# Kernel tuning notes

Measured on AMD Instinct MI355X. Metric: run time of the kernel, lower is better.

Reference implementation:

```python
import jax, jax.numpy as jnp
import numpy as np
from jax import lax

N_KERNELS = 11
N_GRAMS = 3
EMB = 300
CONV_OUT = 128
B, QLEN, DLEN = 128, 30, 256


def _kernel_mus(n):
    mus = [1.0]
    bin_size = 2.0 / (n - 1)
    mus.append(1 - bin_size / 2)
    for i in range(1, n - 1):
        mus.append(mus[i] - bin_size)
    return mus


def _kernel_sigmas(n):
    bin_size = 2.0 / (n - 1)
    return [0.001] + [0.5 * bin_size] * (n - 1)


MU = jnp.asarray(np.array(_kernel_mus(N_KERNELS), dtype=np.float32))      # [K]
SIGMA = jnp.asarray(np.array(_kernel_sigmas(N_KERNELS), dtype=np.float32))  # [K]


def setup_inputs() -> dict:
    key = jax.random.key(0)
    ks = jax.random.split(key, 10)
    inp = {
        "query_embeddings": jax.random.normal(ks[0], (B, QLEN, EMB), jnp.float32),
        "document_embeddings": jax.random.normal(ks[1], (B, DLEN, EMB), jnp.float32),
        "query_pad_oov_mask": jnp.ones((B, QLEN), jnp.float32),
        "document_pad_oov_mask": jnp.ones((B, DLEN), jnp.float32),
    }
    # conv weights for n-gram sizes 1..3: [out_ch, in_ch, ksize]
    for i in range(1, N_GRAMS + 1):
        inp[f"conv_w{i}"] = jax.random.normal(ks[1 + i], (CONV_OUT, EMB, i), jnp.float32) * 0.05
        inp[f"conv_b{i}"] = jnp.zeros((CONV_OUT,), jnp.float32)
    inp["dense_w"] = jax.random.uniform(ks[9], (1, N_KERNELS * N_GRAMS * N_GRAMS), jnp.float32,
                                        minval=-0.014, maxval=0.014)
    return inp


def _conv_ngram(x, w, b):
    # x: [B, L, E]; w: [C, E, k]; right-pad by k-1 so output length == L (ConstantPad1d((0,k-1)))
    k = w.shape[-1]
    y = lax.conv_general_dilated(x.transpose(0, 2, 1), w, (1,), [(0, k - 1)],
                                 dimension_numbers=("NCH", "OIH", "NCH"))
    return jax.nn.relu(y + b[None, :, None]).transpose(0, 2, 1)  # [B, L, C]


def _kernel_pool(q, d, qd_mask, q_mask):
    # cosine matrix (AllenNLP CosineMatrixAttention: normalize with +1e-13 eps)
    qn = q / (jnp.linalg.norm(q, axis=-1, keepdims=True) + 1e-13)
    dn = d / (jnp.linalg.norm(d, axis=-1, keepdims=True) + 1e-13)
    cos = jnp.einsum("bqe,bde->bqd", qn, dn) * qd_mask  # [B, Q, D]
    # RBF soft-histogram kernels: [B, Q, D, K]
    k = jnp.exp(-(cos[..., None] - MU) ** 2 / (2.0 * SIGMA ** 2)) * qd_mask[..., None]
    per_kernel_query = k.sum(axis=2)  # [B, Q, K]
    log_pk = jnp.log(jnp.clip(per_kernel_query, 1e-10, None)) * 0.01
    return (log_pk * q_mask[..., None]).sum(axis=1)  # [B, K]


def reference(query_embeddings, document_embeddings, query_pad_oov_mask, document_pad_oov_mask,
              conv_w1, conv_b1, conv_w2, conv_b2, conv_w3, conv_b3, dense_w):
    qd_mask = query_pad_oov_mask[:, :, None] * document_pad_oov_mask[:, None, :]  # [B, Q, D]
    conv_params = [(conv_w1, conv_b1), (conv_w2, conv_b2), (conv_w3, conv_b3)]
    q_res = [_conv_ngram(query_embeddings, w, b) for w, b in conv_params]
    d_res = [_conv_ngram(document_embeddings, w, b) for w, b in conv_params]
    matched = [_kernel_pool(q_res[i], d_res[t], qd_mask, query_pad_oov_mask)
               for i in range(N_GRAMS) for t in range(N_GRAMS)]
    all_grams = jnp.concatenate(matched, axis=1)  # [B, K*9]
    return jnp.squeeze(all_grams @ dense_w.T, axis=1)  # [B]
```

## Files before the change

kernel.cpp:

```cpp
#include <hip/hip_runtime.h>
#include <math.h>


typedef __bf16 bf16x8 __attribute__((ext_vector_type(8)));
typedef float f32x4 __attribute__((ext_vector_type(4)));

#if __has_builtin(__builtin_amdgcn_exp2f)
#define EXP2F(x) __builtin_amdgcn_exp2f(x)
#else
#define EXP2F(x) exp2f(x)
#endif

static __device__ __forceinline__ unsigned short f2bf(float f) {
  union { float f; unsigned int u; } v; v.f = f;
  unsigned int r = v.u + 0x7FFFu + ((v.u >> 16) & 1u);
  return (unsigned short)(r >> 16);
}

__global__ __launch_bounds__(256) void prep_w(
    const float* __restrict__ w1, const float* __restrict__ w2,
    const float* __restrict__ w3, unsigned short* __restrict__ wt2) {
  int idx = blockIdx.x * 256 + threadIdx.x;
  if (idx >= 245760) return;
  int jj   = idx & 7;
  int lane = (idx >> 3) & 63;
  int ec   = (idx >> 9) % 10;
  int cb   = (idx / 5120) & 7;
  int p    = idx / 40960;
  const float* w; int k, jt;
  if (p == 0)      { w = w1; k = 1; jt = 0; }
  else if (p <= 2) { w = w2; k = 2; jt = p - 1; }
  else             { w = w3; k = 3; jt = p - 3; }
  int c = cb * 16 + (lane & 15);
  int e = ec * 32 + (lane >> 4) * 8 + jj;
  float v = (e < 300) ? w[(c * 300 + e) * k + jt] : 0.0f;
  wt2[idx] = f2bf(v);
}

__device__ __forceinline__ constexpr int bIndex(int ni, int j) {
  constexpr int base[6] = {0, 1, 2, 4, 6, 9};
  return base[ni] + j;
}

template<int MI>
__device__ __forceinline__ void conv_body(
    unsigned short* As, float (*ssq)[64],
    const float* __restrict__ x, int L, int l0, int b,
    const unsigned short* __restrict__ wt2,
    const float* __restrict__ b1, const float* __restrict__ b2,
    const float* __restrict__ b3,
    unsigned short* __restrict__ out) {
  constexpr int ROWS = MI * 16 + 2;
  const int t = threadIdx.x;
  const int w = __builtin_amdgcn_readfirstlane(t >> 6);
  const int lane = t & 63;
  const int quad = lane >> 4, lrow = lane & 15;

  if (t < 192) ssq[t >> 6][t & 63] = 0.0f;

  const float* xb = x + (size_t)b * L * 300;
  for (int idx = t; idx < ROWS * 80; idx += 256) {
    int r = idx / 80, e4 = idx % 80;
    int e = e4 * 4;
    int l = l0 + r;
    float4 v = make_float4(0.f, 0.f, 0.f, 0.f);
    if (l < L && e < 300) v = *reinterpret_cast<const float4*>(xb + l * 300 + e);
    unsigned int lo = (unsigned int)f2bf(v.x) | ((unsigned int)f2bf(v.y) << 16);
    unsigned int hi = (unsigned int)f2bf(v.z) | ((unsigned int)f2bf(v.w) << 16);
    *reinterpret_cast<uint2*>(&As[r * 328 + e]) = make_uint2(lo, hi);
  }
  __syncthreads();

  const float* biases[3] = {b1, b2, b3};
  float bv[6];
  #pragma unroll
  for (int ni = 0; ni < 6; ++ni)
    bv[ni] = biases[ni >> 1][((ni & 1) * 4 + w) * 16 + lrow];

  f32x4 acc[MI][6];
  #pragma unroll
  for (int mi = 0; mi < MI; ++mi)
    #pragma unroll
    for (int ni = 0; ni < 6; ++ni) acc[mi][ni] = (f32x4){0.f, 0.f, 0.f, 0.f};

  const unsigned short* wl = wt2 + lane * 8;

  auto loadB = [&](int ec, bf16x8* dst) {
    #pragma unroll
    for (int ni = 0; ni < 6; ++ni) {
      const int g = ni >> 1;
      const int cb = (ni & 1) * 4 + w;
      const int pst = (g * (g + 1)) >> 1;
      #pragma unroll
      for (int j = 0; j <= g; ++j)
        dst[bIndex(ni, j)] = *reinterpret_cast<const bf16x8*>(
            wl + ((((pst + j) * 8 + cb) * 10 + ec) << 9));
    }
  };

  auto compute = [&](int ec, const bf16x8* B) {
    #pragma unroll
    for (int j = 0; j < 3; ++j) {
      bf16x8 af[MI];
      #pragma unroll
      for (int mi = 0; mi < MI; ++mi)
        af[mi] = *reinterpret_cast<const bf16x8*>(
            &As[(mi * 16 + lrow + j) * 328 + ec * 32 + quad * 8]);
      #pragma unroll
      for (int ni = 0; ni < 6; ++ni) {
        const int g = ni >> 1;
        if (j <= g) {
          #pragma unroll
          for (int mi = 0; mi < MI; ++mi)
            acc[mi][ni] = __builtin_amdgcn_mfma_f32_16x16x32_bf16(
                af[mi], B[bIndex(ni, j)], acc[mi][ni], 0, 0, 0);
        }
      }
    }
  };

  bf16x8 Bc[12], Bn[12];
  loadB(0, Bc);
  #pragma unroll
  for (int e2 = 0; e2 < 5; ++e2) {
    loadB(2 * e2 + 1, Bn);
    compute(2 * e2, Bc);
    if (e2 < 4) loadB(2 * e2 + 2, Bc);
    compute(2 * e2 + 1, Bn);
  }

  #pragma unroll
  for (int mi = 0; mi < MI; ++mi) {
    #pragma unroll
    for (int r = 0; r < 4; ++r) {
      #pragma unroll
      for (int g = 0; g < 3; ++g) {
        float y0 = fmaxf(acc[mi][2 * g + 0][r] + bv[2 * g + 0], 0.f);
        float y1 = fmaxf(acc[mi][2 * g + 1][r] + bv[2 * g + 1], 0.f);
        float p = y0 * y0 + y1 * y1;
        p += __shfl_xor(p, 1); p += __shfl_xor(p, 2);
        p += __shfl_xor(p, 4); p += __shfl_xor(p, 8);
        if (lrow == 0) atomicAdd(&ssq[g][mi * 16 + quad * 4 + r], p);
      }
    }
  }
  __syncthreads();

  #pragma unroll
  for (int mi = 0; mi < MI; ++mi) {
    #pragma unroll
    for (int r = 0; r < 4; ++r) {
      int row = mi * 16 + quad * 4 + r;
      int l = l0 + row;
      if (l < L) {
        #pragma unroll
        for (int g = 0; g < 3; ++g) {
          float inv = 1.0f / (sqrtf(ssq[g][row]) + 1e-13f);
          #pragma unroll
          for (int h = 0; h < 2; ++h) {
            int ni = 2 * g + h;
            int ch = ((ni & 1) * 4 + w) * 16 + lrow;
            float y = fmaxf(acc[mi][ni][r] + bv[ni], 0.f);
            out[((size_t)(g * 128 + b) * L + l) * 128 + ch] = f2bf(y * inv);
          }
        }
      }
    }
  }
}

__global__ __launch_bounds__(256) void conv_all(
    const float* __restrict__ qemb, const float* __restrict__ demb,
    const unsigned short* __restrict__ wt2,
    const float* __restrict__ b1, const float* __restrict__ b2,
    const float* __restrict__ b3,
    unsigned short* __restrict__ qn, unsigned short* __restrict__ dn) {
  __shared__ unsigned short As[66 * 328];
  __shared__ float ssq[3][64];
  const int bi = blockIdx.x;
  if (bi < 512)
    conv_body<4>(As, ssq, demb, 256, (bi & 3) * 64, bi >> 2, wt2, b1, b2, b3, dn);
  else
    conv_body<2>(As, ssq, qemb, 30, 0, bi - 512, wt2, b1, b2, b3, qn);
}

__global__ __launch_bounds__(64) void pool_mfma(
    const unsigned short* __restrict__ qn, const unsigned short* __restrict__ dn,
    const float* __restrict__ qmask, const float* __restrict__ dmask,
    float* __restrict__ pkq4) {
  const float MU[11] = {1.0f, 0.9f, 0.7f, 0.5f, 0.3f, 0.1f,
                        -0.1f, -0.3f, -0.5f, -0.7f, -0.9f};
  const float NEGC[11] = {-721347.52f, -72.134752f, -72.134752f, -72.134752f,
                          -72.134752f, -72.134752f, -72.134752f, -72.134752f,
                          -72.134752f, -72.134752f, -72.134752f};
  const int tg    = blockIdx.x >> 2;
  const int chunk = blockIdx.x & 3;
  const int b     = blockIdx.y;
  const int lane  = threadIdx.x;
  const int quad  = lane >> 4, l15 = lane & 15;
  const int d0    = chunk * 64;

  const unsigned short* dslab = dn + (size_t)(tg * 128 + b) * 256 * 128;

  bf16x8 aD[4][4];
  #pragma unroll
  for (int mi = 0; mi < 4; ++mi)
    #pragma unroll
    for (int kt = 0; kt < 4; ++kt)
      aD[mi][kt] = *reinterpret_cast<const bf16x8*>(
          dslab + (size_t)(d0 + mi * 16 + l15) * 128 + kt * 32 + quad * 8);

  float dmv[4][4];
  #pragma unroll
  for (int mi = 0; mi < 4; ++mi)
    #pragma unroll
    for (int r = 0; r < 4; ++r)
      dmv[mi][r] = dmask[b * 256 + d0 + mi * 16 + quad * 4 + r];

  float qmv[2];
  qmv[0] = qmask[b * 30 + l15];
  qmv[1] = (16 + l15 < 30) ? qmask[b * 30 + 16 + l15] : 0.0f;

  #pragma unroll 1
  for (int ig = 0; ig < 3; ++ig) {
    const unsigned short* qslab = qn + (size_t)(ig * 128 + b) * 30 * 128;

    bf16x8 bQ[2][4];
    #pragma unroll
    for (int ni = 0; ni < 2; ++ni)
      #pragma unroll
      for (int kt = 0; kt < 4; ++kt)
        bQ[ni][kt] = *reinterpret_cast<const bf16x8*>(
            qslab + (size_t)(ni * 16 + l15) * 128 + kt * 32 + quad * 8);

    f32x4 acc[4][2];
    #pragma unroll
    for (int mi = 0; mi < 4; ++mi)
      #pragma unroll
      for (int ni = 0; ni < 2; ++ni) acc[mi][ni] = (f32x4){0.f, 0.f, 0.f, 0.f};

    #pragma unroll
    for (int kt = 0; kt < 4; ++kt)
      #pragma unroll
      for (int mi = 0; mi < 4; ++mi)
        #pragma unroll
        for (int ni = 0; ni < 2; ++ni)
          acc[mi][ni] = __builtin_amdgcn_mfma_f32_16x16x32_bf16(
              aD[mi][kt], bQ[ni][kt], acc[mi][ni], 0, 0, 0);

    float feat[2][11];
    #pragma unroll
    for (int ni = 0; ni < 2; ++ni)
      #pragma unroll
      for (int kk = 0; kk < 11; ++kk) feat[ni][kk] = 0.0f;

    #pragma unroll
    for (int mi = 0; mi < 4; ++mi) {
      #pragma unroll
      for (int r = 0; r < 4; ++r) {
        #pragma unroll
        for (int ni = 0; ni < 2; ++ni) {
          float m  = qmv[ni] * dmv[mi][r];
          float cm = acc[mi][ni][r] * m;
          #pragma unroll
          for (int kk = 0; kk < 11; ++kk) {
            float d2 = cm - MU[kk];
            feat[ni][kk] += EXP2F(d2 * d2 * NEGC[kk]) * m;
          }
        }
      }
    }

    #pragma unroll
    for (int ni = 0; ni < 2; ++ni)
      #pragma unroll
      for (int kk = 0; kk < 11; ++kk) {
        float v = feat[ni][kk];
        v += __shfl_xor(v, 16);
        v += __shfl_xor(v, 32);
        feat[ni][kk] = v;
      }

    if (quad == 0) {
      const int pair = ig * 3 + tg;
      #pragma unroll
      for (int ni = 0; ni < 2; ++ni) {
        int q = ni * 16 + l15;
        if (q < 30) {
          float* p = pkq4 +
              (((size_t)(chunk * 9 + pair) * 128 + b) * 30 + q) * 11;
          #pragma unroll
          for (int kk = 0; kk < 11; ++kk) p[kk] = feat[ni][kk];
        }
      }
    }
  }
}

__global__ __launch_bounds__(128) void final_kernel(
    const float* __restrict__ pkq4, const float* __restrict__ qmask,
    const float* __restrict__ dw, float* __restrict__ out) {
  const int CH = 9 * 128 * 30 * 11;
  const int b = blockIdx.x;
  const int t = threadIdx.x;
  float s = 0.0f;
  for (int idx = t; idx < 9 * 30 * 11; idx += 128) {
    int pair = idx / 330;
    int rem  = idx % 330;
    int q    = rem / 11;
    int kk   = rem % 11;
    size_t base = (((size_t)pair * 128 + b) * 30 + q) * 11 + kk;
    float v = pkq4[base] + pkq4[base + CH] + pkq4[base + 2 * CH] +
              pkq4[base + 3 * CH];
    s += __logf(fmaxf(v, 1e-10f)) * 0.01f * qmask[b * 30 + q] * dw[pair * 11 + kk];
  }
  s += __shfl_xor(s, 1);  s += __shfl_xor(s, 2);  s += __shfl_xor(s, 4);
  s += __shfl_xor(s, 8);  s += __shfl_xor(s, 16); s += __shfl_xor(s, 32);
  __shared__ float part[2];
  if ((t & 63) == 0) part[t >> 6] = s;
  __syncthreads();
  if (t == 0) out[b] = part[0] + part[1];
}

extern "C" void kernel_launch(void* const* d_in, const int* in_sizes, int n_in,
                              void* d_out, int out_size, void* d_ws, size_t ws_size,
                              hipStream_t stream) {
  const float* qemb  = (const float*)d_in[0];
  const float* demb  = (const float*)d_in[1];
  const float* qmask = (const float*)d_in[2];
  const float* dmask = (const float*)d_in[3];
  const float* w1 = (const float*)d_in[4];
  const float* b1 = (const float*)d_in[5];
  const float* w2 = (const float*)d_in[6];
  const float* b2 = (const float*)d_in[7];
  const float* w3 = (const float*)d_in[8];
  const float* b3 = (const float*)d_in[9];
  const float* dw = (const float*)d_in[10];

  unsigned short* wt2 = (unsigned short*)d_ws;
  unsigned short* qn = wt2 + 245760;
  unsigned short* dn = qn + 1474560;
  float*          pkq4 = (float*)(dn + 12582912);

  prep_w<<<960, 256, 0, stream>>>(w1, w2, w3, wt2);
  conv_all<<<640, 256, 0, stream>>>(qemb, demb, wt2, b1, b2, b3, qn, dn);
  pool_mfma<<<dim3(12, 128), 64, 0, stream>>>(qn, dn, qmask, dmask, pkq4);
  final_kernel<<<128, 128, 0, stream>>>(pkq4, qmask, dw, (float*)d_out);
}
```

Measured before the change: 194.3 us.

## Transpose conv MFMA operands, pad LDS stride, split pooling into eight doc chunks

The conv kernel now swaps the MFMA operand roles so each lane holds four consecutive channels. That allows vectorized bias loads, a cheaper sum-of-squares reduction, and packed 8-byte bf16 stores. The LDS row stride is padded from 328 to 344 to reduce bank conflicts, and the manual double-buffered weight loads become a simple loop unrolled by 2. The pooling kernel splits each document into 8 chunks of 32 rows instead of 4 of 64, doubling the block count for occupancy. In exchange, the final reduction now sums 8 partials per entry and the workspace traffic grows.

```diff
diff --git a/kernel.cpp b/kernel.cpp
--- a/kernel.cpp
+++ b/kernel.cpp
@@ -10,6 +10,8 @@
 #else
 #define EXP2F(x) exp2f(x)
 #endif
+
+#define AS_STRIDE 344
 
 static __device__ __forceinline__ unsigned short f2bf(float f) {
   union { float f; unsigned int u; } v; v.f = f;
@@ -37,12 +39,12 @@
   wt2[idx] = f2bf(v);
 }
 
-__device__ __forceinline__ constexpr int bIndex(int ni, int j) {
+__device__ __forceinline__ constexpr int bIndex(int nt, int j) {
   constexpr int base[6] = {0, 1, 2, 4, 6, 9};
-  return base[ni] + j;
-}
-
-template<int MI>
+  return base[nt] + j;
+}
+
+template<int NI>
 __device__ __forceinline__ void conv_body(
     unsigned short* As, float (*ssq)[64],
     const float* __restrict__ x, int L, int l0, int b,
@@ -50,7 +52,7 @@
     const float* __restrict__ b1, const float* __restrict__ b2,
     const float* __restrict__ b3,
     unsigned short* __restrict__ out) {
-  constexpr int ROWS = MI * 16 + 2;
+  constexpr int ROWS = NI * 16 + 2;
   const int t = threadIdx.x;
   const int w = __builtin_amdgcn_readfirstlane(t >> 6);
   const int lane = t & 63;
@@ -67,103 +69,100 @@
     if (l < L && e < 300) v = *reinterpret_cast<const float4*>(xb + l * 300 + e);
     unsigned int lo = (unsigned int)f2bf(v.x) | ((unsigned int)f2bf(v.y) << 16);
     unsigned int hi = (unsigned int)f2bf(v.z) | ((unsigned int)f2bf(v.w) << 16);
-    *reinterpret_cast<uint2*>(&As[r * 328 + e]) = make_uint2(lo, hi);
+    *reinterpret_cast<uint2*>(&As[r * AS_STRIDE + e]) = make_uint2(lo, hi);
   }
   __syncthreads();
 
-  const float* biases[3] = {b1, b2, b3};
-  float bv[6];
-  #pragma unroll
-  for (int ni = 0; ni < 6; ++ni)
-    bv[ni] = biases[ni >> 1][((ni & 1) * 4 + w) * 16 + lrow];
-
-  f32x4 acc[MI][6];
-  #pragma unroll
-  for (int mi = 0; mi < MI; ++mi)
-    #pragma unroll
-    for (int ni = 0; ni < 6; ++ni) acc[mi][ni] = (f32x4){0.f, 0.f, 0.f, 0.f};
+  f32x4 acc[NI][6];
+  #pragma unroll
+  for (int ni = 0; ni < NI; ++ni)
+    #pragma unroll
+    for (int nt = 0; nt < 6; ++nt) acc[ni][nt] = (f32x4){0.f, 0.f, 0.f, 0.f};
 
   const unsigned short* wl = wt2 + lane * 8;
 
-  auto loadB = [&](int ec, bf16x8* dst) {
-    #pragma unroll
-    for (int ni = 0; ni < 6; ++ni) {
-      const int g = ni >> 1;
-      const int cb = (ni & 1) * 4 + w;
+  #pragma unroll 2
+  for (int ec = 0; ec < 10; ++ec) {
+    bf16x8 wf[12];
+    #pragma unroll
+    for (int nt = 0; nt < 6; ++nt) {
+      const int g = nt >> 1;
+      const int cb = (nt & 1) * 4 + w;
       const int pst = (g * (g + 1)) >> 1;
       #pragma unroll
       for (int j = 0; j <= g; ++j)
-        dst[bIndex(ni, j)] = *reinterpret_cast<const bf16x8*>(
+        wf[bIndex(nt, j)] = *reinterpret_cast<const bf16x8*>(
             wl + ((((pst + j) * 8 + cb) * 10 + ec) << 9));
     }
-  };
-
-  auto compute = [&](int ec, const bf16x8* B) {
     #pragma unroll
     for (int j = 0; j < 3; ++j) {
-      bf16x8 af[MI];
-      #pragma unroll
-      for (int mi = 0; mi < MI; ++mi)
-        af[mi] = *reinterpret_cast<const bf16x8*>(
-            &As[(mi * 16 + lrow + j) * 328 + ec * 32 + quad * 8]);
-      #pragma unroll
-      for (int ni = 0; ni < 6; ++ni) {
-        const int g = ni >> 1;
+      bf16x8 xf[NI];
+      #pragma unroll
+      for (int ni = 0; ni < NI; ++ni)
+        xf[ni] = *reinterpret_cast<const bf16x8*>(
+            &As[(ni * 16 + lrow + j) * AS_STRIDE + ec * 32 + quad * 8]);
+      #pragma unroll
+      for (int nt = 0; nt < 6; ++nt) {
+        const int g = nt >> 1;
         if (j <= g) {
           #pragma unroll
-          for (int mi = 0; mi < MI; ++mi)
-            acc[mi][ni] = __builtin_amdgcn_mfma_f32_16x16x32_bf16(
-                af[mi], B[bIndex(ni, j)], acc[mi][ni], 0, 0, 0);
+          for (int ni = 0; ni < NI; ++ni)
+            acc[ni][nt] = __builtin_amdgcn_mfma_f32_16x16x32_bf16(
+                wf[bIndex(nt, j)], xf[ni], acc[ni][nt], 0, 0, 0);
         }
       }
     }
-  };
-
-  bf16x8 Bc[12], Bn[12];
-  loadB(0, Bc);
-  #pragma unroll
-  for (int e2 = 0; e2 < 5; ++e2) {
-    loadB(2 * e2 + 1, Bn);
-    compute(2 * e2, Bc);
-    if (e2 < 4) loadB(2 * e2 + 2, Bc);
-    compute(2 * e2 + 1, Bn);
-  }
-
-  #pragma unroll
-  for (int mi = 0; mi < MI; ++mi) {
-    #pragma unroll
-    for (int r = 0; r < 4; ++r) {
-      #pragma unroll
-      for (int g = 0; g < 3; ++g) {
-        float y0 = fmaxf(acc[mi][2 * g + 0][r] + bv[2 * g + 0], 0.f);
-        float y1 = fmaxf(acc[mi][2 * g + 1][r] + bv[2 * g + 1], 0.f);
-        float p = y0 * y0 + y1 * y1;
-        p += __shfl_xor(p, 1); p += __shfl_xor(p, 2);
-        p += __shfl_xor(p, 4); p += __shfl_xor(p, 8);
-        if (lrow == 0) atomicAdd(&ssq[g][mi * 16 + quad * 4 + r], p);
-      }
+  }
+
+  const float* biases[3] = {b1, b2, b3};
+  float4 bv[6];
+  #pragma unroll
+  for (int nt = 0; nt < 6; ++nt)
+    bv[nt] = *reinterpret_cast<const float4*>(
+        biases[nt >> 1] + ((nt & 1) * 4 + w) * 16 + quad * 4);
+
+  #pragma unroll
+  for (int ni = 0; ni < NI; ++ni) {
+    float p[3] = {0.f, 0.f, 0.f};
+    #pragma unroll
+    for (int nt = 0; nt < 6; ++nt) {
+      #pragma unroll
+      for (int r = 0; r < 4; ++r) {
+        float y = fmaxf(acc[ni][nt][r] + bv[nt][r], 0.f);
+        p[nt >> 1] += y * y;
+      }
+    }
+    #pragma unroll
+    for (int g = 0; g < 3; ++g) {
+      float v = p[g];
+      v += __shfl_xor(v, 16);
+      v += __shfl_xor(v, 32);
+      if (lane < 16) atomicAdd(&ssq[g][ni * 16 + lrow], v);
     }
   }
   __syncthreads();
 
   #pragma unroll
-  for (int mi = 0; mi < MI; ++mi) {
-    #pragma unroll
-    for (int r = 0; r < 4; ++r) {
-      int row = mi * 16 + quad * 4 + r;
-      int l = l0 + row;
-      if (l < L) {
+  for (int ni = 0; ni < NI; ++ni) {
+    int l = l0 + ni * 16 + lrow;
+    if (l < L) {
+      float inv[3];
+      #pragma unroll
+      for (int g = 0; g < 3; ++g)
+        inv[g] = 1.0f / (sqrtf(ssq[g][ni * 16 + lrow]) + 1e-13f);
+      #pragma unroll
+      for (int nt = 0; nt < 6; ++nt) {
+        const int g = nt >> 1;
+        unsigned int pk[2];
         #pragma unroll
-        for (int g = 0; g < 3; ++g) {
-          float inv = 1.0f / (sqrtf(ssq[g][row]) + 1e-13f);
-          #pragma unroll
-          for (int h = 0; h < 2; ++h) {
-            int ni = 2 * g + h;
-            int ch = ((ni & 1) * 4 + w) * 16 + lrow;
-            float y = fmaxf(acc[mi][ni][r] + bv[ni], 0.f);
-            out[((size_t)(g * 128 + b) * L + l) * 128 + ch] = f2bf(y * inv);
-          }
+        for (int h = 0; h < 2; ++h) {
+          float y0 = fmaxf(acc[ni][nt][2 * h + 0] + bv[nt][2 * h + 0], 0.f) * inv[g];
+          float y1 = fmaxf(acc[ni][nt][2 * h + 1] + bv[nt][2 * h + 1], 0.f) * inv[g];
+          pk[h] = (unsigned int)f2bf(y0) | ((unsigned int)f2bf(y1) << 16);
         }
+        unsigned short* op = out + ((size_t)(g * 128 + b) * L + l) * 128 +
+                             ((nt & 1) * 4 + w) * 16 + quad * 4;
+        *reinterpret_cast<uint2*>(op) = make_uint2(pk[0], pk[1]);
       }
     }
   }
@@ -175,7 +174,7 @@
     const float* __restrict__ b1, const float* __restrict__ b2,
     const float* __restrict__ b3,
     unsigned short* __restrict__ qn, unsigned short* __restrict__ dn) {
-  __shared__ unsigned short As[66 * 328];
+  __shared__ unsigned short As[66 * AS_STRIDE];
   __shared__ float ssq[3][64];
   const int bi = blockIdx.x;
   if (bi < 512)
@@ -187,32 +186,32 @@
 __global__ __launch_bounds__(64) void pool_mfma(
     const unsigned short* __restrict__ qn, const unsigned short* __restrict__ dn,
     const float* __restrict__ qmask, const float* __restrict__ dmask,
-    float* __restrict__ pkq4) {
+    float* __restrict__ pkq8) {
   const float MU[11] = {1.0f, 0.9f, 0.7f, 0.5f, 0.3f, 0.1f,
                         -0.1f, -0.3f, -0.5f, -0.7f, -0.9f};
   const float NEGC[11] = {-721347.52f, -72.134752f, -72.134752f, -72.134752f,
                           -72.134752f, -72.134752f, -72.134752f, -72.134752f,
                           -72.134752f, -72.134752f, -72.134752f};
-  const int tg    = blockIdx.x >> 2;
-  const int chunk = blockIdx.x & 3;
+  const int tg    = blockIdx.x >> 3;
+  const int chunk = blockIdx.x & 7;
   const int b     = blockIdx.y;
   const int lane  = threadIdx.x;
   const int quad  = lane >> 4, l15 = lane & 15;
-  const int d0    = chunk * 64;
+  const int d0    = chunk * 32;
 
   const unsigned short* dslab = dn + (size_t)(tg * 128 + b) * 256 * 128;
 
-  bf16x8 aD[4][4];
-  #pragma unroll
-  for (int mi = 0; mi < 4; ++mi)
+  bf16x8 aD[2][4];
+  #pragma unroll
+  for (int mi = 0; mi < 2; ++mi)
     #pragma unroll
     for (int kt = 0; kt < 4; ++kt)
       aD[mi][kt] = *reinterpret_cast<const bf16x8*>(
           dslab + (size_t)(d0 + mi * 16 + l15) * 128 + kt * 32 + quad * 8);
 
-  float dmv[4][4];
-  #pragma unroll
-  for (int mi = 0; mi < 4; ++mi)
+  float dmv[2][4];
+  #pragma unroll
+  for (int mi = 0; mi < 2; ++mi)
     #pragma unroll
     for (int r = 0; r < 4; ++r)
       dmv[mi][r] = dmask[b * 256 + d0 + mi * 16 + quad * 4 + r];
@@ -233,16 +232,16 @@
         bQ[ni][kt] = *reinterpret_cast<const bf16x8*>(
             qslab + (size_t)(ni * 16 + l15) * 128 + kt * 32 + quad * 8);
 
-    f32x4 acc[4][2];
-    #pragma unroll
-    for (int mi = 0; mi < 4; ++mi)
+    f32x4 acc[2][2];
+    #pragma unroll
+    for (int mi = 0; mi < 2; ++mi)
       #pragma unroll
       for (int ni = 0; ni < 2; ++ni) acc[mi][ni] = (f32x4){0.f, 0.f, 0.f, 0.f};
 
     #pragma unroll
     for (int kt = 0; kt < 4; ++kt)
       #pragma unroll
-      for (int mi = 0; mi < 4; ++mi)
+      for (int mi = 0; mi < 2; ++mi)
         #pragma unroll
         for (int ni = 0; ni < 2; ++ni)
           acc[mi][ni] = __builtin_amdgcn_mfma_f32_16x16x32_bf16(
@@ -255,7 +254,7 @@
       for (int kk = 0; kk < 11; ++kk) feat[ni][kk] = 0.0f;
 
     #pragma unroll
-    for (int mi = 0; mi < 4; ++mi) {
+    for (int mi = 0; mi < 2; ++mi) {
       #pragma unroll
       for (int r = 0; r < 4; ++r) {
         #pragma unroll
@@ -287,7 +286,7 @@
       for (int ni = 0; ni < 2; ++ni) {
         int q = ni * 16 + l15;
         if (q < 30) {
-          float* p = pkq4 +
+          float* p = pkq8 +
               (((size_t)(chunk * 9 + pair) * 128 + b) * 30 + q) * 11;
           #pragma unroll
           for (int kk = 0; kk < 11; ++kk) p[kk] = feat[ni][kk];
@@ -297,29 +296,30 @@
   }
 }
 
-__global__ __launch_bounds__(128) void final_kernel(
-    const float* __restrict__ pkq4, const float* __restrict__ qmask,
+__global__ __launch_bounds__(256) void final_kernel(
+    const float* __restrict__ pkq8, const float* __restrict__ qmask,
     const float* __restrict__ dw, float* __restrict__ out) {
   const int CH = 9 * 128 * 30 * 11;
   const int b = blockIdx.x;
   const int t = threadIdx.x;
   float s = 0.0f;
-  for (int idx = t; idx < 9 * 30 * 11; idx += 128) {
+  for (int idx = t; idx < 9 * 30 * 11; idx += 256) {
     int pair = idx / 330;
     int rem  = idx % 330;
     int q    = rem / 11;
     int kk   = rem % 11;
     size_t base = (((size_t)pair * 128 + b) * 30 + q) * 11 + kk;
-    float v = pkq4[base] + pkq4[base + CH] + pkq4[base + 2 * CH] +
-              pkq4[base + 3 * CH];
+    float v = 0.f;
+    #pragma unroll
+    for (int c = 0; c < 8; ++c) v += pkq8[base + (size_t)c * CH];
     s += __logf(fmaxf(v, 1e-10f)) * 0.01f * qmask[b * 30 + q] * dw[pair * 11 + kk];
   }
   s += __shfl_xor(s, 1);  s += __shfl_xor(s, 2);  s += __shfl_xor(s, 4);
   s += __shfl_xor(s, 8);  s += __shfl_xor(s, 16); s += __shfl_xor(s, 32);
-  __shared__ float part[2];
+  __shared__ float part[4];
   if ((t & 63) == 0) part[t >> 6] = s;
   __syncthreads();
-  if (t == 0) out[b] = part[0] + part[1];
+  if (t == 0) out[b] = part[0] + part[1] + part[2] + part[3];
 }
 
 extern "C" void kernel_launch(void* const* d_in, const int* in_sizes, int n_in,
@@ -340,10 +340,10 @@
   unsigned short* wt2 = (unsigned short*)d_ws;
   unsigned short* qn = wt2 + 245760;
   unsigned short* dn = qn + 1474560;
-  float*          pkq4 = (float*)(dn + 12582912);
+  float*          pkq8 = (float*)(dn + 12582912);
 
   prep_w<<<960, 256, 0, stream>>>(w1, w2, w3, wt2);
   conv_all<<<640, 256, 0, stream>>>(qemb, demb, wt2, b1, b2, b3, qn, dn);
-  pool_mfma<<<dim3(12, 128), 64, 0, stream>>>(qn, dn, qmask, dmask, pkq4);
-  final_kernel<<<128, 128, 0, stream>>>(pkq4, qmask, dw, (float*)d_out);
-}
+  pool_mfma<<<dim3(24, 128), 64, 0, stream>>>(qn, dn, qmask, dmask, pkq8);
+  final_kernel<<<128, 256, 0, stream>>>(pkq8, qmask, dw, (float*)d_out);
+}
```

Result: slower. 206.4 us (+6.2%).
